# Kernel optimization log

Measured on AMD Instinct MI355X. Metric: run time of the kernel, lower is better.

Reference implementation:

```python
import jax, jax.numpy as jnp
import numpy as np

D_MODEL = 2048
N_HEADS = 32
N_KV_HEADS = 8
HEAD_DIM = D_MODEL // N_HEADS
N_REP = N_HEADS // N_KV_HEADS
ROPE_BASE = 10000.0


def _rope_tables(seq_len, dim, dtype):
    inv_freq = 1.0 / (ROPE_BASE ** (jnp.arange(0, dim, 2, dtype=jnp.float32) / dim))
    t = jnp.arange(seq_len, dtype=jnp.float32)
    freqs = jnp.einsum('i,j->ij', t, inv_freq)          # [S, dim/2]
    emb = jnp.concatenate([freqs, freqs], axis=-1)      # [S, dim]
    return jnp.cos(emb).astype(dtype), jnp.sin(emb).astype(dtype)


def _apply_rotation(x, cos, sin):
    # x: [B, H, S, D]; cos/sin: [S, D] broadcast over B,H
    half = x.shape[-1] // 2
    x1, x2 = x[..., :half], x[..., half:]
    rot = jnp.concatenate([-x2, x1], axis=-1)
    return rot * sin + x * cos


def setup_inputs() -> dict:
    key = jax.random.key(0)
    kx, kq, kk, kv, ko = jax.random.split(key, 5)
    B, S = 2, 2048
    scale_in = 1.0 / np.sqrt(D_MODEL)
    x = jax.random.normal(kx, (B, S, D_MODEL), dtype=jnp.float32)
    Wq = jax.random.normal(kq, (N_HEADS * HEAD_DIM, D_MODEL), dtype=jnp.float32) * scale_in
    Wk = jax.random.normal(kk, (N_KV_HEADS * HEAD_DIM, D_MODEL), dtype=jnp.float32) * scale_in
    Wv = jax.random.normal(kv, (N_KV_HEADS * HEAD_DIM, D_MODEL), dtype=jnp.float32) * scale_in
    Wo = jax.random.normal(ko, (D_MODEL, N_HEADS * HEAD_DIM), dtype=jnp.float32) * scale_in
    # additive causal mask, broadcast over batch and heads
    neg = jnp.float32(-1e9)
    causal = jnp.triu(jnp.full((S, S), neg, dtype=jnp.float32), k=1)[None, None]
    return {"x": x, "Wq": Wq, "Wk": Wk, "Wv": Wv, "Wo": Wo, "mask": causal}


def reference(x, Wq, Wk, Wv, Wo, mask):
    B, S, _ = x.shape
    q = (x @ Wq.T).reshape(B, S, N_HEADS, HEAD_DIM).transpose(0, 2, 1, 3)      # [B,H,S,D]
    k = (x @ Wk.T).reshape(B, S, N_KV_HEADS, HEAD_DIM).transpose(0, 2, 1, 3)   # [B,Hkv,S,D]
    v = (x @ Wv.T).reshape(B, S, N_KV_HEADS, HEAD_DIM).transpose(0, 2, 1, 3)
    cos, sin = _rope_tables(S, HEAD_DIM, x.dtype)
    q = _apply_rotation(q, cos, sin)
    k = _apply_rotation(k, cos, sin)
    # repeat_kv: [B,Hkv,S,D] -> [B,Hkv*n_rep,S,D]
    k = jnp.repeat(k, N_REP, axis=1)
    v = jnp.repeat(v, N_REP, axis=1)
    scale = jnp.sqrt(jnp.float32(HEAD_DIM)).astype(x.dtype)
    scores = jnp.einsum('bhqd,bhkd->bhqk', q, k) / scale
    scores = scores + mask
    attn = jax.nn.softmax(scores.astype(jnp.float32), axis=-1).astype(q.dtype)
    out = jnp.einsum('bhqk,bhkd->bhqd', attn, v)
    out = out.transpose(0, 2, 1, 3).reshape(B, S, N_HEADS * HEAD_DIM)
    return out @ Wo.T
```

## Files before the change

kernel.cpp:

```cpp
#include <hip/hip_runtime.h>


typedef __bf16 bf16x8 __attribute__((ext_vector_type(8)));
typedef __bf16 bf16x4 __attribute__((ext_vector_type(4)));
typedef float f32x4 __attribute__((ext_vector_type(4)));

__device__ inline f32x4 mfma16(bf16x8 a, bf16x8 b, f32x4 c) {
    return __builtin_amdgcn_mfma_f32_16x16x32_bf16(a, b, c, 0, 0, 0);
}

__device__ inline void gld16(const __bf16* g, __bf16* l) {
    __builtin_amdgcn_global_load_lds(
        (const __attribute__((address_space(1))) void*)g,
        (__attribute__((address_space(3))) void*)l, 16, 0, 0);
}

__device__ inline bf16x4 pk4(float a, float b, float c, float d) {
    bf16x4 r; r[0] = (__bf16)a; r[1] = (__bf16)b; r[2] = (__bf16)c; r[3] = (__bf16)d;
    return r;
}

#define SCALE_Q 0.18033688011112042f
#define L2IF    0.4152410118609203f
#define INV2PI  0.15915494309189535f

__global__ void cvt4_kernel(const float* __restrict__ x,  const float* __restrict__ wq,
                            const float* __restrict__ wk, const float* __restrict__ wv,
                            __bf16* __restrict__ xb, __bf16* __restrict__ wqkvb)
{
    int i = blockIdx.x * blockDim.x + threadIdx.x;
    const float* src; __bf16* dst;
    if (i < 2097152)      { src = x  + (size_t)i * 4;  dst = xb + (size_t)i * 4; }
    else if (i < 3145728) { int j = i - 2097152; src = wq + (size_t)j * 4; dst = wqkvb + (size_t)j * 4; }
    else if (i < 3407872) { int j = i - 3145728; src = wk + (size_t)j * 4; dst = wqkvb + 4194304 + (size_t)j * 4; }
    else                  { int j = i - 3407872; src = wv + (size_t)j * 4; dst = wqkvb + 5242880 + (size_t)j * 4; }
    float4 f = *(const float4*)src;
    *(bf16x4*)dst = pk4(f.x, f.y, f.z, f.w);
}

__global__ void cvt_kernel(const float* __restrict__ in, __bf16* __restrict__ out, int n4)
{
    int i = blockIdx.x * blockDim.x + threadIdx.x;
    if (i >= n4) return;
    float4 f = ((const float4*)in)[i];
    ((bf16x4*)out)[i] = pk4(f.x, f.y, f.z, f.w);
}

#define BK 32

template<bool ROPE, bool OUT_F32>
__global__ __launch_bounds__(256) void gemm_bt(
    const __bf16* __restrict__ A, const __bf16* __restrict__ Bw,
    void* __restrict__ Cv, int M, int N, int K)
{
    __shared__ __bf16 As[128 * BK];
    __shared__ __bf16 Bs[128 * BK];
    const int tid  = threadIdx.x;
    const int lane = tid & 63;
    const int w    = tid >> 6;
    const int lm   = lane & 15;
    const int quad = lane >> 4;
    const int wm   = (w >> 1) * 64;
    const int wn   = (w & 1) * 64;

    int bx, by;
    {
        int id  = blockIdx.x + gridDim.x * blockIdx.y;
        int xcd = id & 7;
        int j   = id >> 3;
        by = xcd * 4 + (j & 3);
        bx = j >> 2;
    }
    const int m0 = by * 128;
    const int n0 = bx * 128;

    f32x4 acc[4][4];
    #pragma unroll
    for (int i = 0; i < 4; ++i)
        #pragma unroll
        for (int j = 0; j < 4; ++j)
            acc[i][j] = (f32x4){0.f, 0.f, 0.f, 0.f};

    const int srow = tid >> 2;
    const int sc8  = (tid & 3) * 8;
    const __bf16* gA0 = A  + (size_t)(m0 + srow) * K + sc8;
    const __bf16* gA1 = gA0 + (size_t)64 * K;
    const __bf16* gB0 = Bw + (size_t)(n0 + srow) * K + sc8;
    const __bf16* gB1 = gB0 + (size_t)64 * K;
    __bf16* lA0 = &As[srow * BK + sc8];
    __bf16* lA1 = &As[(srow + 64) * BK + sc8];
    __bf16* lB0 = &Bs[srow * BK + sc8];
    __bf16* lB1 = &Bs[(srow + 64) * BK + sc8];

    for (int k0 = 0; k0 < K; k0 += BK) {
        gld16(gA0 + k0, lA0);
        gld16(gA1 + k0, lA1);
        gld16(gB0 + k0, lB0);
        gld16(gB1 + k0, lB1);
        __syncthreads();

        bf16x8 af[4], bfr[4];
        #pragma unroll
        for (int i = 0; i < 4; ++i)
            af[i] = *(const bf16x8*)&As[(wm + i * 16 + lm) * BK + quad * 8];
        #pragma unroll
        for (int j = 0; j < 4; ++j)
            bfr[j] = *(const bf16x8*)&Bs[(wn + j * 16 + lm) * BK + quad * 8];
        #pragma unroll
        for (int i = 0; i < 4; ++i)
            #pragma unroll
            for (int j = 0; j < 4; ++j)
                acc[i][j] = mfma16(af[i], bfr[j], acc[i][j]);
        __syncthreads();
    }

    float sc = 1.0f;
    if (ROPE) {
        const int colbase = n0 + wn;
        const int region  = (colbase < 2048) ? 0 : (colbase < 2560 ? 1 : 2);
        if (region < 2) {
            if (region == 0) sc = SCALE_Q;
            float invr[2];
            invr[0] = exp2f(-(float)lm        * L2IF) * INV2PI;
            invr[1] = exp2f(-(float)(16 + lm) * L2IF) * INV2PI;
            #pragma unroll
            for (int i = 0; i < 4; ++i)
                #pragma unroll
                for (int r = 0; r < 4; ++r) {
                    float t = (float)((m0 + wm + i * 16 + quad * 4 + r) & 2047);
                    #pragma unroll
                    for (int jp = 0; jp < 2; ++jp) {
                        float a = t * invr[jp];
                        a -= floorf(a);
                        float cs = __builtin_amdgcn_cosf(a);
                        float sn = __builtin_amdgcn_sinf(a);
                        float x1 = acc[i][jp][r], x2 = acc[i][jp + 2][r];
                        acc[i][jp][r]     = x1 * cs - x2 * sn;
                        acc[i][jp + 2][r] = x2 * cs + x1 * sn;
                    }
                }
        }
    }

    #pragma unroll
    for (int i = 0; i < 4; ++i)
        #pragma unroll
        for (int j = 0; j < 4; ++j)
            #pragma unroll
            for (int r = 0; r < 4; ++r) {
                int row = m0 + wm + i * 16 + quad * 4 + r;
                int col = n0 + wn + j * 16 + lm;
                if (OUT_F32)
                    ((float*)Cv)[(size_t)row * N + col] = acc[i][j][r];
                else
                    ((__bf16*)Cv)[(size_t)row * N + col] = (__bf16)(acc[i][j][r] * sc);
            }
}

__global__ __launch_bounds__(256) void transpose_kernel(
    const __bf16* __restrict__ in, __bf16* __restrict__ out, int rowstride)
{
    __shared__ __bf16 T[64][72];
    const int t0 = blockIdx.x * 64;
    const int d0 = blockIdx.y * 64;
    const int r = threadIdx.x >> 2, c = (threadIdx.x & 3) * 16;
    *(int4*)&T[r][c]     = *(const int4*)(in + (size_t)(t0 + r) * rowstride + d0 + c);
    *(int4*)&T[r][c + 8] = *(const int4*)(in + (size_t)(t0 + r) * rowstride + d0 + c + 8);
    __syncthreads();
    bf16x8 o0, o1;
    #pragma unroll
    for (int i = 0; i < 8; ++i) { o0[i] = T[c + i][r]; o1[i] = T[c + 8 + i][r]; }
    *(bf16x8*)(out + (size_t)(d0 + r) * 4096 + t0 + c)     = o0;
    *(bf16x8*)(out + (size_t)(d0 + r) * 4096 + t0 + c + 8) = o1;
}

#define RS  72
#define PKS 72

__device__ inline void attn_tile(
    const bf16x8 (&qf)[2], f32x4 (&oacc)[4], float& l,
    int qbase, int k0, int w, int lm, int quad,
    const __bf16* Ks, const __bf16* Vs, __bf16* Ptw)
{
    f32x4 st[4];
    #pragma unroll
    for (int n = 0; n < 4; ++n)
        st[n] = (f32x4){0.f, 0.f, 0.f, 0.f};

    #pragma unroll
    for (int n = 0; n < 4; ++n) {
        bf16x8 kf0 = *(const bf16x8*)&Ks[(n * 16 + lm) * RS + quad * 8];
        bf16x8 kf1 = *(const bf16x8*)&Ks[(n * 16 + lm) * RS + 32 + quad * 8];
        st[n] = mfma16(kf0, qf[0], st[n]);
        st[n] = mfma16(kf1, qf[1], st[n]);
    }

    const int qi = qbase + w * 16 + lm;
    const bool any_mask = (k0 + 63 > qbase + w * 16);
    #pragma unroll
    for (int n = 0; n < 4; ++n) {
        const int kv0 = k0 + n * 16 + quad * 4;
        float e0, e1, e2, e3;
        if (any_mask) {
            e0 = (kv0     > qi) ? 0.f : __builtin_amdgcn_exp2f(st[n][0]);
            e1 = (kv0 + 1 > qi) ? 0.f : __builtin_amdgcn_exp2f(st[n][1]);
            e2 = (kv0 + 2 > qi) ? 0.f : __builtin_amdgcn_exp2f(st[n][2]);
            e3 = (kv0 + 3 > qi) ? 0.f : __builtin_amdgcn_exp2f(st[n][3]);
        } else {
            e0 = __builtin_amdgcn_exp2f(st[n][0]); e1 = __builtin_amdgcn_exp2f(st[n][1]);
            e2 = __builtin_amdgcn_exp2f(st[n][2]); e3 = __builtin_amdgcn_exp2f(st[n][3]);
        }
        l += (e0 + e1) + (e2 + e3);
        *(bf16x4*)&Ptw[lm * PKS + n * 16 + quad * 4] = pk4(e0, e1, e2, e3);
    }

    bf16x8 pf0 = *(const bf16x8*)&Ptw[lm * PKS + quad * 8];
    bf16x8 pf1 = *(const bf16x8*)&Ptw[lm * PKS + 32 + quad * 8];
    #pragma unroll
    for (int dt = 0; dt < 4; ++dt) {
        bf16x8 vf0 = *(const bf16x8*)&Vs[(dt * 16 + lm) * RS + quad * 8];
        bf16x8 vf1 = *(const bf16x8*)&Vs[(dt * 16 + lm) * RS + 32 + quad * 8];
        oacc[dt] = mfma16(vf0, pf0, oacc[dt]);
        oacc[dt] = mfma16(vf1, pf1, oacc[dt]);
    }
}

__device__ inline void attn_epilogue(
    f32x4 (&oacc)[4], float l,
    int qbase, int w, int lm, int quad, int b, int h, __bf16* o)
{
    float ls = l;
    ls += __shfl_xor(ls, 16);
    ls += __shfl_xor(ls, 32);
    float rinv = 1.0f / ls;
    const size_t rowbase = (size_t)(b * 2048 + qbase + w * 16 + lm) * 2048 + h * 64;
    #pragma unroll
    for (int dt = 0; dt < 4; ++dt) {
        *(bf16x4*)(o + rowbase + dt * 16 + quad * 4) =
            pk4(oacc[dt][0] * rinv, oacc[dt][1] * rinv,
                oacc[dt][2] * rinv, oacc[dt][3] * rinv);
    }
}

__global__ __launch_bounds__(512) void attn_kernel(
    const __bf16* __restrict__ qkv, const __bf16* __restrict__ vt,
    __bf16* __restrict__ o)
{
    __shared__ __bf16 Ks[2][64 * RS];
    __shared__ __bf16 Vs[2][64 * RS];
    __shared__ __bf16 Pt[8][16 * PKS];
    const int tid  = threadIdx.x;
    const int w    = tid >> 6;
    const int lane = tid & 63;
    const int lm   = lane & 15;
    const int quad = lane >> 4;
    const int p = blockIdx.x, h = blockIdx.y, b = blockIdx.z;
    const int kvh = h >> 2;
    const int qbA = p * 128, qbB = (15 - p) * 128;
    const int ntA = 2 * p + 2, ntB = 32 - 2 * p;
    __bf16* Ptw = &Pt[w][0];

    bf16x8 qfA[2], qfB[2];
    #pragma unroll
    for (int kh = 0; kh < 2; ++kh) {
        qfA[kh] = *(const bf16x8*)(qkv + (size_t)(b * 2048 + qbA + w * 16 + lm) * 3072
                                      + h * 64 + kh * 32 + quad * 8);
        qfB[kh] = *(const bf16x8*)(qkv + (size_t)(b * 2048 + qbB + w * 16 + lm) * 3072
                                      + h * 64 + kh * 32 + quad * 8);
    }

    f32x4 oA[4], oB[4];
    float lA = 0.f, lB = 0.f;
    #pragma unroll
    for (int j = 0; j < 4; ++j) {
        oA[j] = (f32x4){0.f, 0.f, 0.f, 0.f};
        oB[j] = (f32x4){0.f, 0.f, 0.f, 0.f};
    }

    const int srow = tid >> 3;
    const int scol = (tid & 7) * 8;
    const __bf16* kbase = qkv + (size_t)(b * 2048) * 3072 + 2048 + kvh * 64;
    const __bf16* vbase = vt  + (size_t)(kvh * 64 + srow) * 4096 + b * 2048;

    int4 kr0, vr0;
    kr0 = *(const int4*)(kbase + (size_t)srow * 3072 + scol);
    vr0 = *(const int4*)(vbase + scol);

    for (int kt = 0; kt < ntB; ++kt) {
        const int c = kt & 1;
        const int k0 = kt * 64;
        *(int4*)&Ks[c][srow * RS + scol] = kr0;
        *(int4*)&Vs[c][srow * RS + scol] = vr0;
        if (kt + 1 < ntB) {
            kr0 = *(const int4*)(kbase + (size_t)(k0 + 64 + srow) * 3072 + scol);
            vr0 = *(const int4*)(vbase + k0 + 64 + scol);
        }
        __syncthreads();
        attn_tile(qfB, oB, lB, qbB, k0, w, lm, quad, Ks[c], Vs[c], Ptw);
        if (kt < ntA)
            attn_tile(qfA, oA, lA, qbA, k0, w, lm, quad, Ks[c], Vs[c], Ptw);
    }

    attn_epilogue(oA, lA, qbA, w, lm, quad, b, h, o);
    attn_epilogue(oB, lB, qbB, w, lm, quad, b, h, o);
}

extern "C" void kernel_launch(void* const* d_in, const int* in_sizes, int n_in,
                              void* d_out, int out_size, void* d_ws, size_t ws_size,
                              hipStream_t stream)
{
    const float* x  = (const float*)d_in[0];
    const float* Wq = (const float*)d_in[1];
    const float* Wk = (const float*)d_in[2];
    const float* Wv = (const float*)d_in[3];
    const float* Wo = (const float*)d_in[4];

    const size_t Mi = 1u << 20;
    char* ob = (char*)d_out;
    __bf16* xb    = (__bf16*)ob;
    __bf16* wqkvb = (__bf16*)(ob + 16 * Mi);
    __bf16* vt    = (__bf16*)(ob + 28 * Mi);
    char* ws = (char*)d_ws;
    __bf16* qkvc = (__bf16*)ws;
    __bf16* aws  = (__bf16*)(ws + 24 * Mi);
    __bf16* wob  = (__bf16*)ws;

    dim3 blk(256);
    cvt4_kernel<<<14336, blk, 0, stream>>>(x, Wq, Wk, Wv, xb, wqkvb);
    gemm_bt<true, false><<<dim3(24, 32), blk, 0, stream>>>(xb, wqkvb, qkvc, 4096, 3072, 2048);
    transpose_kernel<<<dim3(64, 8), blk, 0, stream>>>(qkvc + 2560, vt, 3072);
    attn_kernel<<<dim3(8, 32, 2), dim3(512), 0, stream>>>(qkvc, vt, aws);
    cvt_kernel<<<4096, blk, 0, stream>>>(Wo, wob, 1048576);
    gemm_bt<false, true><<<dim3(16, 32), blk, 0, stream>>>(aws, wob, d_out, 4096, 2048, 2048);
}
```

Measured before the change: 324.8 us.

## Replace QKV projection GEMM with 256x256 tiled, double-buffered, interleaved-load kernel

Adds a new GEMM kernel with 256x256 output tiles, 512 threads, BK=64, XOR-swizzled LDS layout, and double-buffered global-to-LDS loads interleaved with MFMA phases under explicit waitcnt/barrier/setprio scheduling. It also applies a grid swizzle for L2 locality and fuses RoPE plus Q scaling into the epilogue. It is used only for the fused QKV projection, aiming to raise MFMA utilisation and data reuse over the 128x128 kernel. In exchange the grid is small (192 blocks) and the hand-tuned waitcnt counts make correctness fragile.

```diff
diff --git a/kernel.cpp b/kernel.cpp
--- a/kernel.cpp
+++ b/kernel.cpp
@@ -44,6 +44,191 @@
     if (i >= n4) return;
     float4 f = ((const float4*)in)[i];
     ((bf16x4*)out)[i] = pk4(f.x, f.y, f.z, f.w);
+}
+
+template<bool ROPE, bool OUT_F32>
+__global__ __launch_bounds__(512, 2) void gemm256(
+    const __bf16* __restrict__ A, const __bf16* __restrict__ Bw,
+    void* __restrict__ Cv, int M, int N, int K)
+{
+    __shared__ __bf16 LA[2][16384];
+    __shared__ __bf16 LB[2][16384];
+    const int tid  = threadIdx.x;
+    const int lane = tid & 63;
+    const int w    = tid >> 6;
+    const int lm   = lane & 15;
+    const int quad = lane >> 4;
+    const int wr   = w >> 2;
+    const int wc   = w & 3;
+
+    int bx, by;
+    {
+        int nwg = gridDim.x * gridDim.y;
+        int id  = blockIdx.x + gridDim.x * blockIdx.y;
+        int q   = nwg >> 3;
+        int swz = (id & 7) * q + (id >> 3);
+        by = swz / gridDim.x;
+        bx = swz - by * gridDim.x;
+    }
+    const int m0 = by * 256;
+    const int n0 = bx * 256;
+    const int NT = K >> 6;
+
+    const int srow = tid >> 3;
+    const int scol = ((tid & 7) ^ (srow & 7)) * 8;
+    const int ldst = tid * 8;
+    const __bf16* ga = A  + (size_t)(m0 + srow) * K + scol;
+    const __bf16* gb = Bw + (size_t)(n0 + srow) * K + scol;
+
+    auto STA = [&](int bf, int r, int u) {
+        gld16(ga + (size_t)r * K + u * 64, &LA[bf][r * 64 + ldst]);
+    };
+    auto STB = [&](int bf, int r, int u) {
+        gld16(gb + (size_t)r * K + u * 64, &LB[bf][r * 64 + ldst]);
+    };
+
+    f32x4 acc[8][4];
+    #pragma unroll
+    for (int i = 0; i < 8; ++i)
+        #pragma unroll
+        for (int j = 0; j < 4; ++j)
+            acc[i][j] = (f32x4){0.f, 0.f, 0.f, 0.f};
+
+    const int axo = (wr * 128 + lm) * 64;
+    const int bxo = (wc * 64  + lm) * 64;
+    const int ks0 = ((quad * 8)      ^ ((lm & 7) * 8));
+    const int ks1 = ((32 + quad * 8) ^ ((lm & 7) * 8));
+
+    STA(0, 0, 0); STA(0, 64, 0); STA(0, 128, 0); STA(0, 192, 0);
+    STB(0, 0, 0); STB(0, 64, 0); STB(0, 128, 0); STB(0, 192, 0);
+    STA(1, 0, 1); STA(1, 128, 1); STB(1, 0, 1); STA(1, 64, 1); STB(1, 64, 1);
+    asm volatile("s_waitcnt vmcnt(5)" ::: "memory");
+    __builtin_amdgcn_s_barrier();
+    asm volatile("" ::: "memory");
+
+    bf16x8 Af[4][2], Bf[4][2];
+    for (int t = 0; t < NT; ++t) {
+        const int b = t & 1;
+        const __bf16* la = LA[b];
+        const __bf16* lb = LB[b];
+        #pragma unroll
+        for (int mi = 0; mi < 4; ++mi) {
+            Af[mi][0] = *(const bf16x8*)(la + axo + mi * 1024 + ks0);
+            Af[mi][1] = *(const bf16x8*)(la + axo + mi * 1024 + ks1);
+        }
+        #pragma unroll
+        for (int ni = 0; ni < 2; ++ni) {
+            Bf[ni][0] = *(const bf16x8*)(lb + bxo + ni * 1024 + ks0);
+            Bf[ni][1] = *(const bf16x8*)(lb + bxo + ni * 1024 + ks1);
+        }
+        if (t + 1 < NT) { STA(b ^ 1, 192, t + 1); STB(b ^ 1, 128, t + 1); }
+        __builtin_amdgcn_s_barrier();
+        asm volatile("s_waitcnt lgkmcnt(0)" ::: "memory");
+        __builtin_amdgcn_s_setprio(1);
+        #pragma unroll
+        for (int mi = 0; mi < 4; ++mi)
+            #pragma unroll
+            for (int ni = 0; ni < 2; ++ni) {
+                acc[mi][ni] = mfma16(Af[mi][0], Bf[ni][0], acc[mi][ni]);
+                acc[mi][ni] = mfma16(Af[mi][1], Bf[ni][1], acc[mi][ni]);
+            }
+        __builtin_amdgcn_s_setprio(0);
+        __builtin_amdgcn_s_barrier();
+        #pragma unroll
+        for (int ni = 2; ni < 4; ++ni) {
+            Bf[ni][0] = *(const bf16x8*)(lb + bxo + ni * 1024 + ks0);
+            Bf[ni][1] = *(const bf16x8*)(lb + bxo + ni * 1024 + ks1);
+        }
+        if (t + 1 < NT) STB(b ^ 1, 192, t + 1);
+        if (t + 2 < NT) STA(b, 0, t + 2);
+        __builtin_amdgcn_s_barrier();
+        asm volatile("s_waitcnt lgkmcnt(0)" ::: "memory");
+        __builtin_amdgcn_s_setprio(1);
+        #pragma unroll
+        for (int mi = 0; mi < 4; ++mi)
+            #pragma unroll
+            for (int ni = 2; ni < 4; ++ni) {
+                acc[mi][ni] = mfma16(Af[mi][0], Bf[ni][0], acc[mi][ni]);
+                acc[mi][ni] = mfma16(Af[mi][1], Bf[ni][1], acc[mi][ni]);
+            }
+        __builtin_amdgcn_s_setprio(0);
+        __builtin_amdgcn_s_barrier();
+        #pragma unroll
+        for (int mi = 0; mi < 4; ++mi) {
+            Af[mi][0] = *(const bf16x8*)(la + axo + (mi + 4) * 1024 + ks0);
+            Af[mi][1] = *(const bf16x8*)(la + axo + (mi + 4) * 1024 + ks1);
+        }
+        if (t + 2 < NT) { STA(b, 128, t + 2); STB(b, 0, t + 2); }
+        __builtin_amdgcn_s_barrier();
+        asm volatile("s_waitcnt lgkmcnt(0)" ::: "memory");
+        __builtin_amdgcn_s_setprio(1);
+        #pragma unroll
+        for (int mi = 0; mi < 4; ++mi)
+            #pragma unroll
+            for (int ni = 0; ni < 2; ++ni) {
+                acc[mi + 4][ni] = mfma16(Af[mi][0], Bf[ni][0], acc[mi + 4][ni]);
+                acc[mi + 4][ni] = mfma16(Af[mi][1], Bf[ni][1], acc[mi + 4][ni]);
+            }
+        __builtin_amdgcn_s_setprio(0);
+        __builtin_amdgcn_s_barrier();
+        if (t + 2 < NT) { STA(b, 64, t + 2); STB(b, 64, t + 2); }
+        __builtin_amdgcn_s_barrier();
+        __builtin_amdgcn_s_setprio(1);
+        #pragma unroll
+        for (int mi = 0; mi < 4; ++mi)
+            #pragma unroll
+            for (int ni = 2; ni < 4; ++ni) {
+                acc[mi + 4][ni] = mfma16(Af[mi][0], Bf[ni][0], acc[mi + 4][ni]);
+                acc[mi + 4][ni] = mfma16(Af[mi][1], Bf[ni][1], acc[mi + 4][ni]);
+            }
+        __builtin_amdgcn_s_setprio(0);
+        if (t < NT - 2)       asm volatile("s_waitcnt vmcnt(5)" ::: "memory");
+        else if (t == NT - 2) asm volatile("s_waitcnt vmcnt(0)" ::: "memory");
+        __builtin_amdgcn_s_barrier();
+        asm volatile("" ::: "memory");
+    }
+
+    float sc = 1.0f;
+    if (ROPE) {
+        const int colbase = n0 + wc * 64;
+        const int region  = (colbase < 2048) ? 0 : (colbase < 2560 ? 1 : 2);
+        if (region < 2) {
+            if (region == 0) sc = SCALE_Q;
+            float invr[2];
+            invr[0] = exp2f(-(float)lm        * L2IF) * INV2PI;
+            invr[1] = exp2f(-(float)(16 + lm) * L2IF) * INV2PI;
+            #pragma unroll
+            for (int i = 0; i < 8; ++i)
+                #pragma unroll
+                for (int r = 0; r < 4; ++r) {
+                    float tt = (float)((m0 + wr * 128 + i * 16 + quad * 4 + r) & 2047);
+                    #pragma unroll
+                    for (int jp = 0; jp < 2; ++jp) {
+                        float aR = tt * invr[jp];
+                        aR -= floorf(aR);
+                        float cs = __builtin_amdgcn_cosf(aR);
+                        float sn = __builtin_amdgcn_sinf(aR);
+                        float x1 = acc[i][jp][r], x2 = acc[i][jp + 2][r];
+                        acc[i][jp][r]     = x1 * cs - x2 * sn;
+                        acc[i][jp + 2][r] = x2 * cs + x1 * sn;
+                    }
+                }
+        }
+    }
+
+    #pragma unroll
+    for (int i = 0; i < 8; ++i)
+        #pragma unroll
+        for (int j = 0; j < 4; ++j)
+            #pragma unroll
+            for (int r = 0; r < 4; ++r) {
+                int row = m0 + wr * 128 + i * 16 + quad * 4 + r;
+                int col = n0 + wc * 64 + j * 16 + lm;
+                if (OUT_F32)
+                    ((float*)Cv)[(size_t)row * N + col] = acc[i][j][r];
+                else
+                    ((__bf16*)Cv)[(size_t)row * N + col] = (__bf16)(acc[i][j][r] * sc);
+            }
 }
 
 #define BK 32
@@ -327,7 +512,7 @@
 
     dim3 blk(256);
     cvt4_kernel<<<14336, blk, 0, stream>>>(x, Wq, Wk, Wv, xb, wqkvb);
-    gemm_bt<true, false><<<dim3(24, 32), blk, 0, stream>>>(xb, wqkvb, qkvc, 4096, 3072, 2048);
+    gemm256<true, false><<<dim3(12, 16), dim3(512), 0, stream>>>(xb, wqkvb, qkvc, 4096, 3072, 2048);
     transpose_kernel<<<dim3(64, 8), blk, 0, stream>>>(qkvc + 2560, vt, 3072);
     attn_kernel<<<dim3(8, 32, 2), dim3(512), 0, stream>>>(qkvc, vt, aws);
     cvt_kernel<<<4096, blk, 0, stream>>>(Wo, wob, 1048576);
```

Result: faster. 315.1 us (-3.0%).
